# Kernel optimization log

Hardware: AMD Instinct MI355X
Metric: run time of the kernel (lower is better)

## Reference

```python
import jax, jax.numpy as jnp
import numpy as np

B, T, D, U = 64, 1024, 512, 512
C = D + U  # combined dim
EPS = 1e-3  # keras LayerNormalization default epsilon


def setup_inputs() -> dict:
    key = jax.random.key(0)
    k = jax.random.split(key, 8)
    glorot = jax.nn.initializers.glorot_uniform()
    return {
        "x": jax.random.normal(k[0], (B, T, D), dtype=jnp.float32),
        "h0": jnp.zeros((B, U), dtype=jnp.float32),
        "Wg": glorot(k[1], (C, C), jnp.float32),
        "bg": jnp.zeros((C,), dtype=jnp.float32),
        "Wf": glorot(k[2], (C, U), jnp.float32),
        "bf": jnp.zeros((U,), dtype=jnp.float32),
        "gamma": jnp.ones((U,), dtype=jnp.float32),
        "beta": jnp.zeros((U,), dtype=jnp.float32),
    }


def reference(x, h0, Wg, bg, Wf, bf, gamma, beta):
    """FGRU cell scanned over time. x: [B,T,D] -> out: [B,T,U]."""

    def step(h, xt):  # h: [B,U], xt: [B,D]
        combined = jnp.concatenate([xt, h], axis=-1)          # [B, C]
        gate = jax.nn.sigmoid(combined @ Wg + bg)             # [B, C]
        z = (combined * gate) @ Wf + bf                       # [B, U]
        z = jax.nn.silu(z)
        # LayerNorm over last axis (keras default eps=1e-3)
        mu = jnp.mean(z, axis=-1, keepdims=True)
        var = jnp.mean(jnp.square(z - mu), axis=-1, keepdims=True)
        z = (z - mu) * jax.lax.rsqrt(var + EPS) * gamma + beta
        return z, z

    xs = jnp.swapaxes(x, 0, 1)                                # [T,B,D]
    _, ys = jax.lax.scan(step, h0, xs)                        # [T,B,U]
    return jnp.swapaxes(ys, 0, 1)                             # [B,T,U]
```

## Files before the change

### kernel.cpp

```cpp
#include <hip/hip_runtime.h>
#include <stdint.h>

#define NB 64
#define NT 1024
#define ND 512
#define NU 512
#define NC 1024
#define NWG 64
#define GJ 16
#define ZJ 8

typedef __attribute__((ext_vector_type(8))) short bf16x8;
typedef __attribute__((ext_vector_type(4))) float f32x4;

__device__ __forceinline__ short f2bf(float f) {
  union { float f; uint32_t u; } v; v.f = f;
  uint32_t r = (v.u + 0x7fffu + ((v.u >> 16) & 1u)) >> 16;
  return (short)(uint16_t)r;
}
__device__ __forceinline__ float bf2f(short s) {
  union { uint32_t u; float f; } v; v.u = ((uint32_t)(uint16_t)s) << 16;
  return v.f;
}
__device__ __forceinline__ float sigm(float x) { return 1.0f / (1.0f + __expf(-x)); }

struct SMem {
  short wgx[GJ * 512];
  short wgz[GJ * 512];
  short wf[ZJ * 1024];
  float gamma_s[NU];
  float beta_s[NU];
  float bfv_s[NU];
  float bg_s[GJ];
  float kb_s[GJ];
  float kg_s[GJ];
  float mu_s[NB];
  float rs_s[NB];
  float red[NB][4][2];
  float red2[GJ][16][2];
};

__device__ __forceinline__ void gbar(uint32_t* root, uint32_t* leaf, unsigned ep) {
  __syncthreads();
  if (threadIdx.x == 0) {
    unsigned old = __hip_atomic_fetch_add(leaf, 1u, __ATOMIC_ACQ_REL, __HIP_MEMORY_SCOPE_AGENT);
    if (old == ep * 8u - 1u) {
      __hip_atomic_fetch_add(root, 1u, __ATOMIC_ACQ_REL, __HIP_MEMORY_SCOPE_AGENT);
    }
    while (__hip_atomic_load(root, __ATOMIC_ACQUIRE, __HIP_MEMORY_SCOPE_AGENT) < ep * 8u) {
      __builtin_amdgcn_s_sleep(2);
    }
  }
  __syncthreads();
}

__global__ void __launch_bounds__(256) fgru_init(const float* __restrict__ h0,
    const float* __restrict__ gamma, const float* __restrict__ beta,
    short* __restrict__ z_g, float* __restrict__ stats, uint32_t* __restrict__ bar) {
  int idx = blockIdx.x * 256 + threadIdx.x;
  if (idx < NB * NU) {
    int c = idx & (NU - 1);
    float g = gamma[c];
    if (g == 0.0f) g = 1.0f;
    z_g[idx] = f2bf((h0[idx] - beta[c]) / g);
  }
  if (idx < NB * NWG) {
    int jj = idx & 63;
    stats[idx * 2 + 0] = 0.0f;
    stats[idx * 2 + 1] = (jj == 0) ? (float)NU * (1.0f - 1e-3f) : 0.0f;
  }
  if (idx < 512) bar[idx] = 0u;
}

__global__ void __launch_bounds__(256) fgru_main(
    const float* __restrict__ x, const float* __restrict__ Wg,
    const float* __restrict__ bg, const float* __restrict__ Wf,
    const float* __restrict__ bfv, const float* __restrict__ gamma,
    const float* __restrict__ beta, float* __restrict__ out,
    short* __restrict__ u_g, short* __restrict__ z_g,
    float* __restrict__ stats, uint32_t* __restrict__ bar) {
  __shared__ SMem sm;
  const int j = blockIdx.x;
  const int tid = threadIdx.x;
  const int l = tid & 63;
  const int w = tid >> 6;
  const int lk8 = (l >> 4) * 8;
  const int ncol = l & 15;
  const int swzn = (ncol & 7) << 3;
  const int mrow = w * 16 + (l & 15);

  for (int i = tid; i < NU; i += 256) {
    sm.gamma_s[i] = gamma[i];
    sm.beta_s[i] = beta[i];
    sm.bfv_s[i] = bfv[i];
  }
  if (tid < GJ) sm.bg_s[tid] = bg[j * GJ + tid];
  __syncthreads();
  for (int i = tid; i < GJ * 512; i += 256) {
    int n = i >> 9, k = i & 511;
    int cg = j * GJ + n;
    int dst = n * 512 + (k ^ ((n & 7) << 3));
    sm.wgx[dst] = f2bf(Wg[(size_t)k * NC + cg]);
    sm.wgz[dst] = f2bf(sm.gamma_s[k] * Wg[(size_t)(512 + k) * NC + cg]);
  }
  for (int i = tid; i < ZJ * 1024; i += 256) {
    int n = i >> 10, k = i & 1023;
    int dst = n * 1024 + (k ^ ((n & 7) << 3));
    sm.wf[dst] = f2bf(Wf[(size_t)k * NU + j * ZJ + n]);
  }
  {
    int n = tid >> 4, part = tid & 15;
    float sb = 0.f, sg = 0.f;
    int cg = j * GJ + n;
    for (int k = part * 32; k < part * 32 + 32; ++k) {
      float wv = Wg[(size_t)(512 + k) * NC + cg];
      sb += sm.beta_s[k] * wv;
      sg += sm.gamma_s[k] * wv;
    }
    sm.red2[n][part][0] = sb;
    sm.red2[n][part][1] = sg;
  }
  __syncthreads();
  if (tid < GJ) {
    float sb = 0.f, sg = 0.f;
    #pragma unroll
    for (int p = 0; p < 16; ++p) { sb += sm.red2[tid][p][0]; sg += sm.red2[tid][p][1]; }
    sm.kb_s[tid] = sb;
    sm.kg_s[tid] = sg;
  }
  __syncthreads();

  uint32_t* root = bar;
  uint32_t* leaf = bar + 32 + (j >> 3) * 32;
  unsigned ep = 0;

  for (int t = 0; t <= NT; ++t) {
    {
      int row = tid >> 2, part = tid & 3;
      float s1 = 0.f, s2 = 0.f;
      const float* sp = &stats[row * 128 + part * 32];
      #pragma unroll
      for (int q2 = 0; q2 < 16; ++q2) { s1 += sp[q2 * 2]; s2 += sp[q2 * 2 + 1]; }
      sm.red[row][part][0] = s1;
      sm.red[row][part][1] = s2;
    }
    __syncthreads();
    if (tid < NB) {
      float s1 = 0.f, s2 = 0.f;
      #pragma unroll
      for (int p = 0; p < 4; ++p) { s1 += sm.red[tid][p][0]; s2 += sm.red[tid][p][1]; }
      float mu = s1 * (1.0f / NU);
      float var = s2 * (1.0f / NU) - mu * mu;
      sm.mu_s[tid] = mu;
      sm.rs_s[tid] = rsqrtf(var + 1e-3f);
    }
    __syncthreads();

    if (t > 0) {
      for (int e = tid; e < NB * ZJ; e += 256) {
        int row = e >> 3, c = e & 7;
        int col = j * ZJ + c;
        float zv = bf2f(z_g[row * NU + col]);
        float hv = (zv - sm.mu_s[row]) * sm.rs_s[row] * sm.gamma_s[col] + sm.beta_s[col];
        out[(size_t)row * NT * NU + (size_t)(t - 1) * NU + col] = hv;
      }
    }
    if (t == NT) break;

    f32x4 accX = {0.f, 0.f, 0.f, 0.f};
    f32x4 accZ = {0.f, 0.f, 0.f, 0.f};
    const float* xrow = &x[(size_t)mrow * NT * ND + (size_t)t * ND];
    #pragma unroll 4
    for (int ks = 0; ks < 16; ++ks) {
      int k0 = ks * 32 + lk8;
      f32x4 xa = *(const f32x4*)(xrow + k0);
      f32x4 xb = *(const f32x4*)(xrow + k0 + 4);
      bf16x8 a;
      a[0] = f2bf(xa[0]); a[1] = f2bf(xa[1]); a[2] = f2bf(xa[2]); a[3] = f2bf(xa[3]);
      a[4] = f2bf(xb[0]); a[5] = f2bf(xb[1]); a[6] = f2bf(xb[2]); a[7] = f2bf(xb[3]);
      bf16x8 wx = *(const bf16x8*)&sm.wgx[ncol * 512 + (k0 ^ swzn)];
      accX = __builtin_amdgcn_mfma_f32_16x16x32_bf16(a, wx, accX, 0, 0, 0);
      bf16x8 az = *(const bf16x8*)&z_g[mrow * NU + k0];
      bf16x8 wz = *(const bf16x8*)&sm.wgz[ncol * 512 + (k0 ^ swzn)];
      accZ = __builtin_amdgcn_mfma_f32_16x16x32_bf16(az, wz, accZ, 0, 0, 0);
    }
    {
      int cg = j * GJ + ncol;
      float kbv = sm.kb_s[ncol], kgv = sm.kg_s[ncol], bgv = sm.bg_s[ncol];
      #pragma unroll
      for (int q = 0; q < 4; ++q) {
        int r = w * 16 + (l >> 4) * 4 + q;
        float mu = sm.mu_s[r], rs = sm.rs_s[r];
        float g = sigm(accX[q] + rs * accZ[q] + kbv - mu * rs * kgv + bgv);
        float comb;
        if (cg < ND) {
          comb = x[(size_t)r * NT * ND + (size_t)t * ND + cg];
        } else {
          int c = cg - ND;
          float zv = bf2f(z_g[r * NU + c]);
          comb = (zv - mu) * rs * sm.gamma_s[c] + sm.beta_s[c];
        }
        u_g[r * NC + cg] = f2bf(comb * g);
      }
    }

    ++ep;
    gbar(root, leaf, ep);

    f32x4 acc = {0.f, 0.f, 0.f, 0.f};
    #pragma unroll 4
    for (int ks = 0; ks < 32; ++ks) {
      int k0 = ks * 32 + lk8;
      bf16x8 a = *(const bf16x8*)&u_g[mrow * NC + k0];
      bf16x8 b;
      if (ncol < ZJ) {
        b = *(const bf16x8*)&sm.wf[ncol * 1024 + (k0 ^ swzn)];
      } else {
        b[0]=0;b[1]=0;b[2]=0;b[3]=0;b[4]=0;b[5]=0;b[6]=0;b[7]=0;
      }
      acc = __builtin_amdgcn_mfma_f32_16x16x32_bf16(a, b, acc, 0, 0, 0);
    }
    #pragma unroll
    for (int q = 0; q < 4; ++q) {
      int r = w * 16 + (l >> 4) * 4 + q;
      float sv = 0.f, sq = 0.f;
      if (ncol < ZJ) {
        int col = j * ZJ + ncol;
        float zraw = acc[q] + sm.bfv_s[col];
        float s = zraw * sigm(zraw);
        z_g[r * NU + col] = f2bf(s);
        sv = s;
        sq = s * s;
      }
      sv += __shfl_xor(sv, 1); sq += __shfl_xor(sq, 1);
      sv += __shfl_xor(sv, 2); sq += __shfl_xor(sq, 2);
      sv += __shfl_xor(sv, 4); sq += __shfl_xor(sq, 4);
      if (ncol == 0) {
        stats[r * 128 + j * 2 + 0] = sv;
        stats[r * 128 + j * 2 + 1] = sq;
      }
    }

    ++ep;
    gbar(root, leaf, ep);
  }
}

extern "C" void kernel_launch(void* const* d_in, const int* in_sizes, int n_in,
                              void* d_out, int out_size, void* d_ws, size_t ws_size,
                              hipStream_t stream) {
  const float* x     = (const float*)d_in[0];
  const float* h0    = (const float*)d_in[1];
  const float* Wg    = (const float*)d_in[2];
  const float* bg    = (const float*)d_in[3];
  const float* Wf    = (const float*)d_in[4];
  const float* bfv   = (const float*)d_in[5];
  const float* gamma = (const float*)d_in[6];
  const float* beta  = (const float*)d_in[7];
  float* out = (float*)d_out;

  char* ws = (char*)d_ws;
  uint32_t* bar = (uint32_t*)ws;
  short* u_g    = (short*)(ws + 2048);
  short* z_g    = (short*)(ws + 2048 + NB * NC * 2);
  float* stats  = (float*)(ws + 2048 + NB * NC * 2 + NB * NU * 2);

  fgru_init<<<128, 256, 0, stream>>>(h0, gamma, beta, z_g, stats, bar);
  fgru_main<<<NWG, 256, 0, stream>>>(x, Wg, bg, Wf, bfv, gamma, beta, out,
                                     u_g, z_g, stats, bar);
}
```

Measured before the change: 26.72 ms.

## Prefetch next-step x during barrier and batch cross-block loads with relaxed atomics

Restructures the persistent recurrent loop. The next timestep's x tile is prefetched and converted to bf16 while the grid barrier is pending. Each block stages its u and z outputs in LDS and publishes them as packed 8-byte relaxed atomic stores. All cross-block loads of z, stats and u are issued up front into registers before the MFMA loops. Weights are pre-laid out in MFMA fragment order so no swizzle is needed, and the final output row is handled after the loop. The aim is to shorten the serial per-step critical path, at the cost of heavy register pressure and a memory-ordering scheme that depends on relaxed atomics plus the barrier being sufficient for correctness.

```diff
diff --git a/kernel.cpp b/kernel.cpp
--- a/kernel.cpp
+++ b/kernel.cpp
@@ -12,6 +12,7 @@
 
 typedef __attribute__((ext_vector_type(8))) short bf16x8;
 typedef __attribute__((ext_vector_type(4))) float f32x4;
+typedef unsigned long long u64;
 
 __device__ __forceinline__ short f2bf(float f) {
   union { float f; uint32_t u; } v; v.f = f;
@@ -24,10 +25,30 @@
 }
 __device__ __forceinline__ float sigm(float x) { return 1.0f / (1.0f + __expf(-x)); }
 
+__device__ __forceinline__ u64 ald8(const void* p) {
+  return __hip_atomic_load((const u64*)p, __ATOMIC_RELAXED, __HIP_MEMORY_SCOPE_AGENT);
+}
+__device__ __forceinline__ void ast8(void* p, u64 v) {
+  __hip_atomic_store((u64*)p, v, __ATOMIC_RELAXED, __HIP_MEMORY_SCOPE_AGENT);
+}
+__device__ __forceinline__ bf16x8 ald16(const short* p) {
+  union { bf16x8 v; u64 q[2]; } u;
+  u.q[0] = ald8(p);
+  u.q[1] = ald8(p + 4);
+  return u.v;
+}
+__device__ __forceinline__ unsigned ald4(const uint32_t* p) {
+  return __hip_atomic_load(p, __ATOMIC_RELAXED, __HIP_MEMORY_SCOPE_AGENT);
+}
+__device__ __forceinline__ unsigned afadd(uint32_t* p) {
+  return __hip_atomic_fetch_add(p, 1u, __ATOMIC_RELAXED, __HIP_MEMORY_SCOPE_AGENT);
+}
+
 struct SMem {
-  short wgx[GJ * 512];
-  short wgz[GJ * 512];
-  short wf[ZJ * 1024];
+  short wgx[16 * 512];
+  short wgz[16 * 512];
+  short wf[32 * 512];
+  short u_s[NB * GJ];
   float gamma_s[NU];
   float beta_s[NU];
   float bfv_s[NU];
@@ -36,23 +57,10 @@
   float kg_s[GJ];
   float mu_s[NB];
   float rs_s[NB];
+  float z_s[NB * ZJ];
   float red[NB][4][2];
   float red2[GJ][16][2];
 };
-
-__device__ __forceinline__ void gbar(uint32_t* root, uint32_t* leaf, unsigned ep) {
-  __syncthreads();
-  if (threadIdx.x == 0) {
-    unsigned old = __hip_atomic_fetch_add(leaf, 1u, __ATOMIC_ACQ_REL, __HIP_MEMORY_SCOPE_AGENT);
-    if (old == ep * 8u - 1u) {
-      __hip_atomic_fetch_add(root, 1u, __ATOMIC_ACQ_REL, __HIP_MEMORY_SCOPE_AGENT);
-    }
-    while (__hip_atomic_load(root, __ATOMIC_ACQUIRE, __HIP_MEMORY_SCOPE_AGENT) < ep * 8u) {
-      __builtin_amdgcn_s_sleep(2);
-    }
-  }
-  __syncthreads();
-}
 
 __global__ void __launch_bounds__(256) fgru_init(const float* __restrict__ h0,
     const float* __restrict__ gamma, const float* __restrict__ beta,
@@ -72,7 +80,7 @@
   if (idx < 512) bar[idx] = 0u;
 }
 
-__global__ void __launch_bounds__(256) fgru_main(
+__global__ void __launch_bounds__(256, 1) fgru_main(
     const float* __restrict__ x, const float* __restrict__ Wg,
     const float* __restrict__ bg, const float* __restrict__ Wf,
     const float* __restrict__ bfv, const float* __restrict__ gamma,
@@ -84,10 +92,11 @@
   const int tid = threadIdx.x;
   const int l = tid & 63;
   const int w = tid >> 6;
-  const int lk8 = (l >> 4) * 8;
+  const int g4 = l >> 4;
   const int ncol = l & 15;
-  const int swzn = (ncol & 7) << 3;
-  const int mrow = w * 16 + (l & 15);
+  const int lk8 = g4 * 8;
+  const int mrow = w * 16 + ncol;
+  const int cg = j * GJ + ncol;
 
   for (int i = tid; i < NU; i += 256) {
     sm.gamma_s[i] = gamma[i];
@@ -96,24 +105,25 @@
   }
   if (tid < GJ) sm.bg_s[tid] = bg[j * GJ + tid];
   __syncthreads();
-  for (int i = tid; i < GJ * 512; i += 256) {
-    int n = i >> 9, k = i & 511;
-    int cg = j * GJ + n;
-    int dst = n * 512 + (k ^ ((n & 7) << 3));
-    sm.wgx[dst] = f2bf(Wg[(size_t)k * NC + cg]);
-    sm.wgz[dst] = f2bf(sm.gamma_s[k] * Wg[(size_t)(512 + k) * NC + cg]);
-  }
-  for (int i = tid; i < ZJ * 1024; i += 256) {
-    int n = i >> 10, k = i & 1023;
-    int dst = n * 1024 + (k ^ ((n & 7) << 3));
-    sm.wf[dst] = f2bf(Wf[(size_t)k * NU + j * ZJ + n]);
+  for (int i = tid; i < 16 * 512; i += 256) {
+    int ks = i >> 9, slot = (i >> 3) & 63, e = i & 7;
+    int gg = slot >> 4, n = slot & 15;
+    int k = ks * 32 + gg * 8 + e;
+    sm.wgx[i] = f2bf(Wg[(size_t)k * NC + j * GJ + n]);
+    sm.wgz[i] = f2bf(sm.gamma_s[k] * Wg[(size_t)(512 + k) * NC + j * GJ + n]);
+  }
+  for (int i = tid; i < 32 * 512; i += 256) {
+    int ks = i >> 9, slot = (i >> 3) & 63, e = i & 7;
+    int gg = slot >> 4, n = slot & 15;
+    int k = ks * 32 + gg * 8 + e;
+    sm.wf[i] = (n < ZJ) ? f2bf(Wf[(size_t)k * NU + j * ZJ + n]) : (short)0;
   }
   {
     int n = tid >> 4, part = tid & 15;
     float sb = 0.f, sg = 0.f;
-    int cg = j * GJ + n;
+    int cgn = j * GJ + n;
     for (int k = part * 32; k < part * 32 + 32; ++k) {
-      float wv = Wg[(size_t)(512 + k) * NC + cg];
+      float wv = Wg[(size_t)(512 + k) * NC + cgn];
       sb += sm.beta_s[k] * wv;
       sg += sm.gamma_s[k] * wv;
     }
@@ -128,21 +138,68 @@
     sm.kb_s[tid] = sb;
     sm.kg_s[tid] = sg;
   }
-  __syncthreads();
 
   uint32_t* root = bar;
   uint32_t* leaf = bar + 32 + (j >> 3) * 32;
   unsigned ep = 0;
 
-  for (int t = 0; t <= NT; ++t) {
+  bf16x8 xa[16];
+  float xcomb[4];
+  auto PFX = [&](int tt) {
+    const float* xr = x + (size_t)mrow * NT * ND + (size_t)tt * ND;
+    #pragma unroll
+    for (int ks = 0; ks < 16; ++ks) {
+      f32x4 p0 = *(const f32x4*)(xr + ks * 32 + lk8);
+      f32x4 p1 = *(const f32x4*)(xr + ks * 32 + lk8 + 4);
+      bf16x8 a;
+      a[0] = f2bf(p0[0]); a[1] = f2bf(p0[1]); a[2] = f2bf(p0[2]); a[3] = f2bf(p0[3]);
+      a[4] = f2bf(p1[0]); a[5] = f2bf(p1[1]); a[6] = f2bf(p1[2]); a[7] = f2bf(p1[3]);
+      xa[ks] = a;
+    }
+    if (cg < ND) {
+      #pragma unroll
+      for (int q = 0; q < 4; ++q)
+        xcomb[q] = x[(size_t)(w * 16 + g4 * 4 + q) * NT * ND + (size_t)tt * ND + cg];
+    }
+  };
+  PFX(0);
+  __syncthreads();
+
+  for (int t = 0; t < NT; ++t) {
+    bf16x8 zr[16];
+    #pragma unroll
+    for (int ks = 0; ks < 16; ++ks)
+      zr[ks] = ald16(z_g + mrow * NU + ks * 32 + lk8);
+    u64 sreg[16];
     {
-      int row = tid >> 2, part = tid & 3;
+      const float* sp = stats + (tid >> 2) * 128 + (tid & 3) * 32;
+      #pragma unroll
+      for (int i2 = 0; i2 < 16; ++i2) sreg[i2] = ald8(sp + i2 * 2);
+    }
+    u64 zc[4];
+    if (cg >= ND) {
+      #pragma unroll
+      for (int q = 0; q < 4; ++q)
+        zc[q] = ald8(z_g + (w * 16 + g4 * 4 + q) * NU + ((cg - ND) & ~3));
+    }
+
+    f32x4 accX = {0.f, 0.f, 0.f, 0.f};
+    f32x4 accZ = {0.f, 0.f, 0.f, 0.f};
+    #pragma unroll
+    for (int ks = 0; ks < 16; ++ks) {
+      bf16x8 wx = *(const bf16x8*)&sm.wgx[ks * 512 + l * 8];
+      bf16x8 wz = *(const bf16x8*)&sm.wgz[ks * 512 + l * 8];
+      accX = __builtin_amdgcn_mfma_f32_16x16x32_bf16(xa[ks], wx, accX, 0, 0, 0);
+      accZ = __builtin_amdgcn_mfma_f32_16x16x32_bf16(zr[ks], wz, accZ, 0, 0, 0);
+    }
+
+    {
+      union { u64 q; float f[2]; } uu;
       float s1 = 0.f, s2 = 0.f;
-      const float* sp = &stats[row * 128 + part * 32];
-      #pragma unroll
-      for (int q2 = 0; q2 < 16; ++q2) { s1 += sp[q2 * 2]; s2 += sp[q2 * 2 + 1]; }
-      sm.red[row][part][0] = s1;
-      sm.red[row][part][1] = s2;
+      #pragma unroll
+      for (int i2 = 0; i2 < 16; ++i2) { uu.q = sreg[i2]; s1 += uu.f[0]; s2 += uu.f[1]; }
+      sm.red[tid >> 2][tid & 3][0] = s1;
+      sm.red[tid >> 2][tid & 3][1] = s2;
     }
     __syncthreads();
     if (tid < NB) {
@@ -157,78 +214,71 @@
     __syncthreads();
 
     if (t > 0) {
-      for (int e = tid; e < NB * ZJ; e += 256) {
-        int row = e >> 3, c = e & 7;
-        int col = j * ZJ + c;
-        float zv = bf2f(z_g[row * NU + col]);
-        float hv = (zv - sm.mu_s[row]) * sm.rs_s[row] * sm.gamma_s[col] + sm.beta_s[col];
-        out[(size_t)row * NT * NU + (size_t)(t - 1) * NU + col] = hv;
+      #pragma unroll
+      for (int e0 = 0; e0 < 2; ++e0) {
+        int e = tid + e0 * 256;
+        int row = e >> 3, c = e & 7, col = j * ZJ + c;
+        out[(size_t)row * NT * NU + (size_t)(t - 1) * NU + col] =
+            (sm.z_s[row * ZJ + c] - sm.mu_s[row]) * sm.rs_s[row] * sm.gamma_s[col] + sm.beta_s[col];
       }
     }
-    if (t == NT) break;
-
-    f32x4 accX = {0.f, 0.f, 0.f, 0.f};
-    f32x4 accZ = {0.f, 0.f, 0.f, 0.f};
-    const float* xrow = &x[(size_t)mrow * NT * ND + (size_t)t * ND];
-    #pragma unroll 4
-    for (int ks = 0; ks < 16; ++ks) {
-      int k0 = ks * 32 + lk8;
-      f32x4 xa = *(const f32x4*)(xrow + k0);
-      f32x4 xb = *(const f32x4*)(xrow + k0 + 4);
-      bf16x8 a;
-      a[0] = f2bf(xa[0]); a[1] = f2bf(xa[1]); a[2] = f2bf(xa[2]); a[3] = f2bf(xa[3]);
-      a[4] = f2bf(xb[0]); a[5] = f2bf(xb[1]); a[6] = f2bf(xb[2]); a[7] = f2bf(xb[3]);
-      bf16x8 wx = *(const bf16x8*)&sm.wgx[ncol * 512 + (k0 ^ swzn)];
-      accX = __builtin_amdgcn_mfma_f32_16x16x32_bf16(a, wx, accX, 0, 0, 0);
-      bf16x8 az = *(const bf16x8*)&z_g[mrow * NU + k0];
-      bf16x8 wz = *(const bf16x8*)&sm.wgz[ncol * 512 + (k0 ^ swzn)];
-      accZ = __builtin_amdgcn_mfma_f32_16x16x32_bf16(az, wz, accZ, 0, 0, 0);
-    }
+
     {
-      int cg = j * GJ + ncol;
       float kbv = sm.kb_s[ncol], kgv = sm.kg_s[ncol], bgv = sm.bg_s[ncol];
       #pragma unroll
       for (int q = 0; q < 4; ++q) {
-        int r = w * 16 + (l >> 4) * 4 + q;
+        int r = w * 16 + g4 * 4 + q;
         float mu = sm.mu_s[r], rs = sm.rs_s[r];
-        float g = sigm(accX[q] + rs * accZ[q] + kbv - mu * rs * kgv + bgv);
+        float gt = sigm(accX[q] + rs * accZ[q] + kbv - mu * rs * kgv + bgv);
         float comb;
         if (cg < ND) {
-          comb = x[(size_t)r * NT * ND + (size_t)t * ND + cg];
+          comb = xcomb[q];
         } else {
+          union { u64 q2; short s4[4]; } uz;
+          uz.q2 = zc[q];
           int c = cg - ND;
-          float zv = bf2f(z_g[r * NU + c]);
+          float zv = bf2f(uz.s4[c & 3]);
           comb = (zv - mu) * rs * sm.gamma_s[c] + sm.beta_s[c];
         }
-        u_g[r * NC + cg] = f2bf(comb * g);
+        sm.u_s[r * GJ + ncol] = f2bf(comb * gt);
       }
     }
+    __syncthreads();
+    ast8(u_g + (tid >> 2) * NC + j * GJ + (tid & 3) * 4, ((const u64*)sm.u_s)[tid]);
 
     ++ep;
-    gbar(root, leaf, ep);
-
-    f32x4 acc = {0.f, 0.f, 0.f, 0.f};
-    #pragma unroll 4
-    for (int ks = 0; ks < 32; ++ks) {
-      int k0 = ks * 32 + lk8;
-      bf16x8 a = *(const bf16x8*)&u_g[mrow * NC + k0];
-      bf16x8 b;
-      if (ncol < ZJ) {
-        b = *(const bf16x8*)&sm.wf[ncol * 1024 + (k0 ^ swzn)];
-      } else {
-        b[0]=0;b[1]=0;b[2]=0;b[3]=0;b[4]=0;b[5]=0;b[6]=0;b[7]=0;
-      }
-      acc = __builtin_amdgcn_mfma_f32_16x16x32_bf16(a, b, acc, 0, 0, 0);
+    __syncthreads();
+    if (tid == 0) {
+      unsigned old = afadd(leaf);
+      if (old == ep * 8u - 1u) afadd(root);
+    }
+    if (t + 1 < NT) PFX(t + 1);
+    if (tid == 0) {
+      while (ald4(root) < ep * 8u) __builtin_amdgcn_s_sleep(1);
+    }
+    __syncthreads();
+
+    bf16x8 ur[32];
+    #pragma unroll
+    for (int ks = 0; ks < 32; ++ks)
+      ur[ks] = ald16(u_g + mrow * NC + ks * 32 + lk8);
+    f32x4 a0 = {0.f, 0.f, 0.f, 0.f};
+    f32x4 a1 = {0.f, 0.f, 0.f, 0.f};
+    #pragma unroll
+    for (int ks = 0; ks < 32; ks += 2) {
+      bf16x8 b0 = *(const bf16x8*)&sm.wf[ks * 512 + l * 8];
+      bf16x8 b1 = *(const bf16x8*)&sm.wf[(ks + 1) * 512 + l * 8];
+      a0 = __builtin_amdgcn_mfma_f32_16x16x32_bf16(ur[ks], b0, a0, 0, 0, 0);
+      a1 = __builtin_amdgcn_mfma_f32_16x16x32_bf16(ur[ks + 1], b1, a1, 0, 0, 0);
     }
     #pragma unroll
     for (int q = 0; q < 4; ++q) {
-      int r = w * 16 + (l >> 4) * 4 + q;
+      int r = w * 16 + g4 * 4 + q;
       float sv = 0.f, sq = 0.f;
       if (ncol < ZJ) {
-        int col = j * ZJ + ncol;
-        float zraw = acc[q] + sm.bfv_s[col];
+        float zraw = a0[q] + a1[q] + sm.bfv_s[j * ZJ + ncol];
         float s = zraw * sigm(zraw);
-        z_g[r * NU + col] = f2bf(s);
+        sm.z_s[r * ZJ + ncol] = s;
         sv = s;
         sq = s * s;
       }
@@ -236,13 +286,61 @@
       sv += __shfl_xor(sv, 2); sq += __shfl_xor(sq, 2);
       sv += __shfl_xor(sv, 4); sq += __shfl_xor(sq, 4);
       if (ncol == 0) {
-        stats[r * 128 + j * 2 + 0] = sv;
-        stats[r * 128 + j * 2 + 1] = sq;
+        union { u64 q2; float f[2]; } pv;
+        pv.f[0] = sv; pv.f[1] = sq;
+        ast8(stats + r * 128 + j * 2, pv.q2);
       }
     }
+    __syncthreads();
+    if (tid < 128) {
+      int row = tid >> 1, b4 = (tid & 1) * 4;
+      union { u64 q2; short s4[4]; } pz;
+      #pragma unroll
+      for (int i2 = 0; i2 < 4; ++i2) pz.s4[i2] = f2bf(sm.z_s[row * ZJ + b4 + i2]);
+      ast8(z_g + row * NU + j * ZJ + b4, pz.q2);
+    }
 
     ++ep;
-    gbar(root, leaf, ep);
+    __syncthreads();
+    if (tid == 0) {
+      unsigned old = afadd(leaf);
+      if (old == ep * 8u - 1u) afadd(root);
+    }
+    if (tid == 0) {
+      while (ald4(root) < ep * 8u) __builtin_amdgcn_s_sleep(1);
+    }
+    __syncthreads();
+  }
+
+  {
+    u64 sreg[16];
+    const float* sp = stats + (tid >> 2) * 128 + (tid & 3) * 32;
+    #pragma unroll
+    for (int i2 = 0; i2 < 16; ++i2) sreg[i2] = ald8(sp + i2 * 2);
+    union { u64 q; float f[2]; } uu;
+    float s1 = 0.f, s2 = 0.f;
+    #pragma unroll
+    for (int i2 = 0; i2 < 16; ++i2) { uu.q = sreg[i2]; s1 += uu.f[0]; s2 += uu.f[1]; }
+    sm.red[tid >> 2][tid & 3][0] = s1;
+    sm.red[tid >> 2][tid & 3][1] = s2;
+    __syncthreads();
+    if (tid < NB) {
+      float a = 0.f, b = 0.f;
+      #pragma unroll
+      for (int p = 0; p < 4; ++p) { a += sm.red[tid][p][0]; b += sm.red[tid][p][1]; }
+      float mu = a * (1.0f / NU);
+      float var = b * (1.0f / NU) - mu * mu;
+      sm.mu_s[tid] = mu;
+      sm.rs_s[tid] = rsqrtf(var + 1e-3f);
+    }
+    __syncthreads();
+    #pragma unroll
+    for (int e0 = 0; e0 < 2; ++e0) {
+      int e = tid + e0 * 256;
+      int row = e >> 3, c = e & 7, col = j * ZJ + c;
+      out[(size_t)row * NT * NU + (size_t)(NT - 1) * NU + col] =
+          (sm.z_s[row * ZJ + c] - sm.mu_s[row]) * sm.rs_s[row] * sm.gamma_s[col] + sm.beta_s[col];
+    }
   }
 }
 
```

After: 23.44 ms. 1.14x faster.
